# Optimization experiments

Measured on AMD Instinct MI355X. Metric: run time of the kernel, lower is better.

## Reference

```python
import jax, jax.numpy as jnp
import numpy as np

N = 50000          # nodes
E = 1600000        # edges (avg degree 32)
IN_C, HID_C, OUT_C = 256, 256, 256


def setup_inputs() -> dict:
    key = jax.random.key(0)
    ks = jax.random.split(key, 10)
    x = jax.random.normal(ks[0], (N, IN_C), dtype=jnp.float32)
    edge_index = jax.random.randint(ks[1], (2, E), 0, N, dtype=jnp.int32)
    edge_weight = jax.random.uniform(ks[2], (E,), dtype=jnp.float32)
    W1 = jax.random.normal(ks[3], (IN_C, HID_C), dtype=jnp.float32) / np.float32(np.sqrt(IN_C))
    b1 = jnp.zeros((HID_C,), dtype=jnp.float32)
    W2 = jax.random.normal(ks[4], (HID_C, OUT_C), dtype=jnp.float32) / np.float32(np.sqrt(HID_C))
    b2 = jnp.zeros((OUT_C,), dtype=jnp.float32)
    Wf = jax.random.normal(ks[5], (OUT_C, 1), dtype=jnp.float32) / np.float32(np.sqrt(OUT_C))
    bf = jnp.zeros((1,), dtype=jnp.float32)
    return {"x": x, "edge_index": edge_index, "edge_weight": edge_weight,
            "W1": W1, "b1": b1, "W2": W2, "b2": b2, "Wf": Wf, "bf": bf}


def _gcn_norm(edge_index, edge_weight, num_nodes, dtype):
    # add self loops with weight 1 (PyG gcn_norm default, add_self_loops=True)
    src, dst = edge_index[0], edge_index[1]
    loop = jnp.arange(num_nodes, dtype=edge_index.dtype)
    src_f = jnp.concatenate([src, loop])
    dst_f = jnpp_concat = jnp.concatenate([dst, loop])
    w_f = jnp.concatenate([edge_weight.astype(dtype), jnp.ones((num_nodes,), dtype)])
    # degree over destination nodes (flow source_to_target)
    deg = jax.ops.segment_sum(w_f, dst_f, num_segments=num_nodes)
    dinv = jnp.where(deg > 0, jax.lax.rsqrt(deg), jnp.array(0.0, dtype))
    norm = dinv[src_f] * w_f * dinv[dst_f]   # [E + N]
    return src_f, dst_f, norm


def _gcn_conv(x, src_f, dst_f, norm, W, b):
    h = x @ W                                    # transform first: [N, out]
    msg = h[src_f] * norm[:, None]               # gather + edge-wise scale: [E+N, out]
    agg = jax.ops.segment_sum(msg, dst_f, num_segments=x.shape[0])  # scatter-add
    return agg + b


def reference(x, edge_index, edge_weight, W1, b1, W2, b2, Wf, bf):
    n = x.shape[0]
    src_f, dst_f, norm = _gcn_norm(edge_index, edge_weight, n, x.dtype)
    h = jax.nn.relu(_gcn_conv(x, src_f, dst_f, norm, W1, b1))
    h = jax.nn.relu(_gcn_conv(h, src_f, dst_f, norm, W2, b2))
    out = h @ Wf + bf
    return out
```

## Files before the change

kernel.cpp:

```cpp
#include <hip/hip_runtime.h>
#include <hip/hip_bf16.h>
#include <cstdint>

#define IN_C 256

typedef __attribute__((ext_vector_type(8))) short bf16x8;
typedef __attribute__((ext_vector_type(8))) short s16x8;
typedef __attribute__((ext_vector_type(4))) short s16x4;
typedef __attribute__((ext_vector_type(8))) unsigned short u16x8;
typedef __attribute__((ext_vector_type(4))) float f32x4;

#define FIXED_SCALE 33554432.0f
#define FIXED_INV   (1.0f / 33554432.0f)
#define DEG_MASK    ((1ULL << 40) - 1)

__device__ inline unsigned short f2bf(float f) {
    union { float f; unsigned int u; } v; v.f = f;
    unsigned int r = (v.u + 0x7fffu + ((v.u >> 16) & 1u)) >> 16;
    return (unsigned short)r;
}
__device__ inline float bf2f(unsigned short b) {
    union { unsigned int u; float f; } v; v.u = ((unsigned int)b) << 16;
    return v.f;
}
__device__ inline short2 split1(float f) {
    unsigned short hb = f2bf(f);
    unsigned short lb = f2bf(f - bf2f(hb));
    return make_short2((short)hb, (short)lb);
}

__global__ void deg_count_kernel(const int* __restrict__ ei, const float* __restrict__ w,
                                 unsigned long long* __restrict__ packed,
                                 unsigned short* __restrict__ rank, int E) {
    int e = blockIdx.x * blockDim.x + threadIdx.x;
    if (e >= E) return;
    int dst = ei[E + e];
    unsigned int fx = __float2uint_rn(w[e] * FIXED_SCALE);
    unsigned long long inc = (1ULL << 40) | (unsigned long long)fx;
    unsigned long long old = atomicAdd(&packed[dst], inc);
    rank[e] = (unsigned short)(old >> 40);
}

#define SCAN_B 256
__global__ void scan1_kernel(const unsigned long long* __restrict__ packed,
                             int* __restrict__ rp, int* __restrict__ bsum,
                             float* __restrict__ dinv, int N) {
    __shared__ int s[SCAN_B];
    int tid = threadIdx.x;
    int i = blockIdx.x * SCAN_B + tid;
    int v = 0;
    if (i < N) {
        unsigned long long pk = packed[i];
        v = (int)(pk >> 40);
        float deg = (float)(pk & DEG_MASK) * FIXED_INV;
        dinv[i] = rsqrtf(deg + 1.0f);
    }
    s[tid] = v;
    __syncthreads();
    for (int off = 1; off < SCAN_B; off <<= 1) {
        int t = (tid >= off) ? s[tid - off] : 0;
        __syncthreads();
        s[tid] += t;
        __syncthreads();
    }
    if (i < N) rp[i] = s[tid] - v;
    if (tid == SCAN_B - 1) bsum[blockIdx.x] = s[tid];
}

__global__ void scan2_kernel(int* __restrict__ bsum, int* __restrict__ boff, int nb) {
    __shared__ int s[SCAN_B];
    int tid = threadIdx.x;
    int v = (tid < nb) ? bsum[tid] : 0;
    s[tid] = v;
    __syncthreads();
    for (int off = 1; off < SCAN_B; off <<= 1) {
        int t = (tid >= off) ? s[tid - off] : 0;
        __syncthreads();
        s[tid] += t;
        __syncthreads();
    }
    if (tid < nb) boff[tid] = s[tid] - v;
}

__global__ void scan3_kernel(int* __restrict__ rp, const int* __restrict__ boff,
                             int N, int E) {
    int i = blockIdx.x * blockDim.x + threadIdx.x;
    if (i < N) rp[i] = rp[i] + boff[i >> 8];
    if (i == 0) rp[N] = E;
}

__global__ void fill_kernel(const int* __restrict__ ei, const float* __restrict__ w,
                            const float* __restrict__ dinv,
                            const int* __restrict__ rp,
                            const unsigned short* __restrict__ rank,
                            int2* __restrict__ cv, int E) {
    int e = blockIdx.x * blockDim.x + threadIdx.x;
    if (e >= E) return;
    int src = ei[e];
    int dst = ei[E + e];
    int pos = rp[dst] + (int)rank[e];
    if ((unsigned)pos < (unsigned)E) {
        float v = dinv[src] * w[e] * dinv[dst];
        cv[pos] = make_int2(src, __float_as_int(v));
    }
}

__global__ void prep_kernel(const float* __restrict__ W1, const float* __restrict__ W2,
                            const float* __restrict__ x,
                            unsigned short* __restrict__ w1t_hi, unsigned short* __restrict__ w1t_lo,
                            unsigned short* __restrict__ w2t_hi, unsigned short* __restrict__ w2t_lo,
                            unsigned short* __restrict__ x_hi, unsigned short* __restrict__ x_lo,
                            int nx4) {
    int b = blockIdx.x;
    if (b < 512) {
        const float* W = (b < 256) ? W1 : W2;
        unsigned short* hi = (b < 256) ? w1t_hi : w2t_hi;
        unsigned short* lo = (b < 256) ? w1t_lo : w2t_lo;
        int n = b & 255;
        int k = threadIdx.x;
        float v = W[(size_t)k * 256 + n];
        short2 s = split1(v);
        hi[(size_t)n * 256 + k] = (unsigned short)s.x;
        lo[(size_t)n * 256 + k] = (unsigned short)s.y;
    } else {
        int i = (b - 512) * 256 + threadIdx.x;
        if (i < nx4) {
            float4 v = ((const float4*)x)[i];
            short2 sx = split1(v.x), sy = split1(v.y), sz = split1(v.z), sw = split1(v.w);
            s16x4 hv, lv;
            hv.x = sx.x; hv.y = sy.x; hv.z = sz.x; hv.w = sw.x;
            lv.x = sx.y; lv.y = sy.y; lv.z = sz.y; lv.w = sw.y;
            *(s16x4*)(x_hi + (size_t)i * 4) = hv;
            *(s16x4*)(x_lo + (size_t)i * 4) = lv;
        }
    }
}

__global__ __launch_bounds__(256) void gemm_split_kernel(
    const unsigned short* __restrict__ Ahg,
    const unsigned short* __restrict__ Alg,
    const unsigned short* __restrict__ Bth,
    const unsigned short* __restrict__ Btl,
    unsigned short* __restrict__ C16, int Nrows)
{
    __shared__ __align__(16) short Ah[128 * 64];
    __shared__ __align__(16) short Al[128 * 64];
    __shared__ __align__(16) short Bh[128 * 64];
    __shared__ __align__(16) short Bl[128 * 64];

    const int t    = threadIdx.x;
    const int lane = t & 63;
    const int w    = t >> 6;
    const int r0   = blockIdx.x * 128;
    const int cb0  = blockIdx.y * 128;
    const int fr   = lane & 15;
    const int fk   = (lane >> 4) * 8;
    const int wm   = w * 32;

    f32x4 acc[2][8] = {};

    for (int k0 = 0; k0 < 256; k0 += 64) {
        __syncthreads();
#pragma unroll
        for (int c = 0; c < 4; ++c) {
            int i = c * 256 + t;
            int row = i >> 3, seg = i & 7;
            size_t g = (size_t)(cb0 + row) * 256 + k0 + seg * 8;
            *(s16x8*)&Bh[row * 64 + seg * 8] = *(const s16x8*)(Bth + g);
            *(s16x8*)&Bl[row * 64 + seg * 8] = *(const s16x8*)(Btl + g);
        }
#pragma unroll
        for (int c = 0; c < 4; ++c) {
            int i = c * 256 + t;
            int row = i >> 3, seg = i & 7;
            int gr = r0 + row; if (gr > Nrows - 1) gr = Nrows - 1;
            size_t g = (size_t)gr * 256 + k0 + seg * 8;
            *(s16x8*)&Ah[row * 64 + seg * 8] = *(const s16x8*)(Ahg + g);
            *(s16x8*)&Al[row * 64 + seg * 8] = *(const s16x8*)(Alg + g);
        }
        __syncthreads();
#pragma unroll
        for (int ks = 0; ks < 2; ++ks) {
            int ko = ks * 32 + fk;
            bf16x8 ah[2], al[2];
#pragma unroll
            for (int mi = 0; mi < 2; ++mi) {
                ah[mi] = *(const bf16x8*)&Ah[(wm + mi * 16 + fr) * 64 + ko];
                al[mi] = *(const bf16x8*)&Al[(wm + mi * 16 + fr) * 64 + ko];
            }
#pragma unroll
            for (int n = 0; n < 8; ++n) {
                bf16x8 bh = *(const bf16x8*)&Bh[(n * 16 + fr) * 64 + ko];
                bf16x8 bl = *(const bf16x8*)&Bl[(n * 16 + fr) * 64 + ko];
#pragma unroll
                for (int mi = 0; mi < 2; ++mi) {
                    acc[mi][n] = __builtin_amdgcn_mfma_f32_16x16x32_bf16(ah[mi], bh, acc[mi][n], 0, 0, 0);
                    acc[mi][n] = __builtin_amdgcn_mfma_f32_16x16x32_bf16(ah[mi], bl, acc[mi][n], 0, 0, 0);
                    acc[mi][n] = __builtin_amdgcn_mfma_f32_16x16x32_bf16(al[mi], bh, acc[mi][n], 0, 0, 0);
                }
            }
        }
    }
    const int rb = (lane >> 4) * 4;
#pragma unroll
    for (int mi = 0; mi < 2; ++mi) {
#pragma unroll
        for (int n = 0; n < 8; ++n) {
            int col = cb0 + n * 16 + fr;
#pragma unroll
            for (int r = 0; r < 4; ++r) {
                int row = r0 + wm + mi * 16 + rb + r;
                if (row < Nrows) C16[(size_t)row * 256 + col] = f2bf(acc[mi][n][r]);
            }
        }
    }
}

__device__ inline void fma8(float* acc, u16x8 g, float v) {
#pragma unroll
    for (int c = 0; c < 8; ++c) acc[c] = fmaf(v, bf2f(g[c]), acc[c]);
}

__global__ __launch_bounds__(256) void agg_kernel(const unsigned short* __restrict__ h16,
                                                  const int* __restrict__ rp,
                                                  const int2* __restrict__ cv,
                                                  const float* __restrict__ dinv,
                                                  const float* __restrict__ bias,
                                                  unsigned short* __restrict__ out_hi,
                                                  unsigned short* __restrict__ out_lo,
                                                  const float* __restrict__ Wf,
                                                  const float* __restrict__ bf,
                                                  float* __restrict__ out,
                                                  int N) {
    int d    = blockIdx.x * 4 + (threadIdx.x >> 6);
    int lane = threadIdx.x & 63;
    if (d >= N) return;
    int half = lane >> 5;
    int co   = (lane & 31) * 8;

    float di = dinv[d];
    float selfm = half ? 0.0f : di * di;
    u16x8 sv = *(const u16x8*)(h16 + (size_t)d * 256 + co);
    float acc[8];
#pragma unroll
    for (int c = 0; c < 8; ++c) acc[c] = selfm * bf2f(sv[c]);

    int s = rp[d], e = rp[d + 1];
    int j = s;
    for (; j + 16 <= e; j += 16) {
        int   ec[8]; float ev[8];
#pragma unroll
        for (int t2 = 0; t2 < 8; ++t2) {
            int2 ca = cv[j + 2 * t2], cb = cv[j + 2 * t2 + 1];
            ec[t2] = half ? cb.x : ca.x;
            ev[t2] = __int_as_float(half ? cb.y : ca.y);
        }
        u16x8 g0 = *(const u16x8*)(h16 + (size_t)ec[0] * 256 + co);
        u16x8 g1 = *(const u16x8*)(h16 + (size_t)ec[1] * 256 + co);
        u16x8 g2 = *(const u16x8*)(h16 + (size_t)ec[2] * 256 + co);
        u16x8 g3 = *(const u16x8*)(h16 + (size_t)ec[3] * 256 + co);
        u16x8 g4 = *(const u16x8*)(h16 + (size_t)ec[4] * 256 + co);
        u16x8 g5 = *(const u16x8*)(h16 + (size_t)ec[5] * 256 + co);
        u16x8 g6 = *(const u16x8*)(h16 + (size_t)ec[6] * 256 + co);
        u16x8 g7 = *(const u16x8*)(h16 + (size_t)ec[7] * 256 + co);
        fma8(acc, g0, ev[0]);
        fma8(acc, g1, ev[1]);
        fma8(acc, g2, ev[2]);
        fma8(acc, g3, ev[3]);
        fma8(acc, g4, ev[4]);
        fma8(acc, g5, ev[5]);
        fma8(acc, g6, ev[6]);
        fma8(acc, g7, ev[7]);
    }
    for (; j + 8 <= e; j += 8) {
        int   ec[4]; float ev[4];
#pragma unroll
        for (int t2 = 0; t2 < 4; ++t2) {
            int2 ca = cv[j + 2 * t2], cb = cv[j + 2 * t2 + 1];
            ec[t2] = half ? cb.x : ca.x;
            ev[t2] = __int_as_float(half ? cb.y : ca.y);
        }
        u16x8 g0 = *(const u16x8*)(h16 + (size_t)ec[0] * 256 + co);
        u16x8 g1 = *(const u16x8*)(h16 + (size_t)ec[1] * 256 + co);
        u16x8 g2 = *(const u16x8*)(h16 + (size_t)ec[2] * 256 + co);
        u16x8 g3 = *(const u16x8*)(h16 + (size_t)ec[3] * 256 + co);
        fma8(acc, g0, ev[0]);
        fma8(acc, g1, ev[1]);
        fma8(acc, g2, ev[2]);
        fma8(acc, g3, ev[3]);
    }
    for (; j + 2 <= e; j += 2) {
        int2 ca = cv[j], cb = cv[j + 1];
        int   ee = half ? cb.x : ca.x;
        float vv = __int_as_float(half ? cb.y : ca.y);
        u16x8 g = *(const u16x8*)(h16 + (size_t)ee * 256 + co);
        fma8(acc, g, vv);
    }
    if (j < e) {
        int2 ca = cv[j];
        int   ee = ca.x;
        float vv = half ? 0.0f : __int_as_float(ca.y);
        u16x8 g = *(const u16x8*)(h16 + (size_t)ee * 256 + co);
        fma8(acc, g, vv);
    }

#pragma unroll
    for (int c = 0; c < 8; ++c) acc[c] += __shfl_xor(acc[c], 32);

    float4 b0 = *(const float4*)(bias + co);
    float4 b1 = *(const float4*)(bias + co + 4);
    acc[0] = fmaxf(acc[0] + b0.x, 0.0f);
    acc[1] = fmaxf(acc[1] + b0.y, 0.0f);
    acc[2] = fmaxf(acc[2] + b0.z, 0.0f);
    acc[3] = fmaxf(acc[3] + b0.w, 0.0f);
    acc[4] = fmaxf(acc[4] + b1.x, 0.0f);
    acc[5] = fmaxf(acc[5] + b1.y, 0.0f);
    acc[6] = fmaxf(acc[6] + b1.z, 0.0f);
    acc[7] = fmaxf(acc[7] + b1.w, 0.0f);

    if (out_hi != nullptr) {
        u16x8 hi;
#pragma unroll
        for (int c = 0; c < 8; ++c) hi[c] = f2bf(acc[c]);
        if (half == 0) {
            *(u16x8*)(out_hi + (size_t)d * 256 + co) = hi;
        } else {
            u16x8 lo;
#pragma unroll
            for (int c = 0; c < 8; ++c) lo[c] = f2bf(acc[c] - bf2f(hi[c]));
            *(u16x8*)(out_lo + (size_t)d * 256 + co) = lo;
        }
    } else {
        float4 wf0 = *(const float4*)(Wf + co);
        float4 wf1 = *(const float4*)(Wf + co + 4);
        float sdot = acc[0] * wf0.x + acc[1] * wf0.y + acc[2] * wf0.z + acc[3] * wf0.w
                   + acc[4] * wf1.x + acc[5] * wf1.y + acc[6] * wf1.z + acc[7] * wf1.w;
        for (int o = 16; o; o >>= 1) sdot += __shfl_down(sdot, o);
        if (lane == 0) out[d] = sdot + bf[0];
    }
}

extern "C" void kernel_launch(void* const* d_in, const int* in_sizes, int n_in,
                              void* d_out, int out_size, void* d_ws, size_t ws_size,
                              hipStream_t stream) {
    const float* x  = (const float*)d_in[0];
    const int*   ei = (const int*)d_in[1];
    const float* w  = (const float*)d_in[2];
    const float* W1 = (const float*)d_in[3];
    const float* b1 = (const float*)d_in[4];
    const float* W2 = (const float*)d_in[5];
    const float* b2 = (const float*)d_in[6];
    const float* Wf = (const float*)d_in[7];
    const float* bf = (const float*)d_in[8];
    float* out = (float*)d_out;

    const int N = in_sizes[0] / IN_C;
    const int E = in_sizes[2];

    auto align256 = [](size_t v) { return (v + 255) & ~(size_t)255; };
    char* p = (char*)d_ws;
    unsigned long long* packed = (unsigned long long*)p; p += align256((size_t)N * 8);
    float* dinv   = (float*)p; p += align256((size_t)N * 4);
    int*   rp     = (int*)p;   p += align256(((size_t)N + 1) * 4);
    int*   bsum   = (int*)p;   p += align256(SCAN_B * 4);
    int*   boff   = (int*)p;   p += align256(SCAN_B * 4);
    unsigned short* rank = (unsigned short*)p; p += align256((size_t)E * 2);
    int2*  cv     = (int2*)p;  p += align256((size_t)E * 8);
    unsigned short* w1t_hi = (unsigned short*)p; p += align256((size_t)256 * 256 * 2);
    unsigned short* w1t_lo = (unsigned short*)p; p += align256((size_t)256 * 256 * 2);
    unsigned short* w2t_hi = (unsigned short*)p; p += align256((size_t)256 * 256 * 2);
    unsigned short* w2t_lo = (unsigned short*)p; p += align256((size_t)256 * 256 * 2);
    unsigned short* hbuf  = (unsigned short*)p; p += align256((size_t)N * 256 * 2);
    unsigned short* xa_hi = (unsigned short*)p; p += align256((size_t)N * 256 * 2);
    unsigned short* xa_lo = (unsigned short*)p; p += align256((size_t)N * 256 * 2);
    (void)ws_size; (void)n_in; (void)out_size;

    const int nb_edges = (E + 255) / 256;
    const int nb_nodes = (N + 255) / 256;
    const int nb_scan  = (N + SCAN_B - 1) / SCAN_B;
    const int nx4      = N * 256 / 4;

    hipMemsetAsync(packed, 0, (size_t)N * 8, stream);

    deg_count_kernel<<<nb_edges, 256, 0, stream>>>(ei, w, packed, rank, E);
    scan1_kernel<<<nb_scan, SCAN_B, 0, stream>>>(packed, rp, bsum, dinv, N);
    scan2_kernel<<<1, SCAN_B, 0, stream>>>(bsum, boff, nb_scan);
    scan3_kernel<<<nb_nodes, 256, 0, stream>>>(rp, boff, N, E);
    fill_kernel<<<nb_edges, 256, 0, stream>>>(ei, w, dinv, rp, rank, cv, E);

    prep_kernel<<<512 + (nx4 + 255) / 256, 256, 0, stream>>>(
        W1, W2, x, w1t_hi, w1t_lo, w2t_hi, w2t_lo, xa_hi, xa_lo, nx4);

    dim3 ggrid((N + 127) / 128, 2);
    const int nb_agg = (N + 3) / 4;

    gemm_split_kernel<<<ggrid, 256, 0, stream>>>(xa_hi, xa_lo, w1t_hi, w1t_lo, hbuf, N);
    agg_kernel<<<nb_agg, 256, 0, stream>>>(hbuf, rp, cv, dinv, b1,
                                           xa_hi, xa_lo, nullptr, nullptr, nullptr, N);
    gemm_split_kernel<<<ggrid, 256, 0, stream>>>(xa_hi, xa_lo, w2t_hi, w2t_lo, hbuf, N);
    agg_kernel<<<nb_agg, 256, 0, stream>>>(hbuf, rp, cv, dinv, b2,
                                           nullptr, nullptr, Wf, bf, out, N);
}
```

Before: 473.4 us.

## Split aggregation into column slices with four lanes per node

The aggregation kernel now gives each node four lanes covering a 32-column slice, with eight slices launched along grid y. Before, a whole wavefront handled one node with two halves over edges. The goal is to keep each column slice of the gathered feature matrix hot in cache across many nodes and to drop the cross-half shuffle reduction. In exchange, the edge list is re-read eight times, tails are padded with zero-weight gathers, and the final head output needs an extra memset plus an atomicAdd per slice.

```diff
diff --git a/kernel.cpp b/kernel.cpp
--- a/kernel.cpp
+++ b/kernel.cpp
@@ -221,6 +221,7 @@
     for (int c = 0; c < 8; ++c) acc[c] = fmaf(v, bf2f(g[c]), acc[c]);
 }
 
+template<int MODE>
 __global__ __launch_bounds__(256) void agg_kernel(const unsigned short* __restrict__ h16,
                                                   const int* __restrict__ rp,
                                                   const int2* __restrict__ cv,
@@ -232,28 +233,28 @@
                                                   const float* __restrict__ bf,
                                                   float* __restrict__ out,
                                                   int N) {
-    int d    = blockIdx.x * 4 + (threadIdx.x >> 6);
-    int lane = threadIdx.x & 63;
+    int q  = threadIdx.x >> 2;
+    int ql = threadIdx.x & 3;
+    int d  = blockIdx.x * 64 + q;
     if (d >= N) return;
-    int half = lane >> 5;
-    int co   = (lane & 31) * 8;
+    int co = blockIdx.y * 32 + ql * 8;
 
     float di = dinv[d];
-    float selfm = half ? 0.0f : di * di;
+    float selfm = di * di;
     u16x8 sv = *(const u16x8*)(h16 + (size_t)d * 256 + co);
     float acc[8];
 #pragma unroll
     for (int c = 0; c < 8; ++c) acc[c] = selfm * bf2f(sv[c]);
 
     int s = rp[d], e = rp[d + 1];
-    int j = s;
-    for (; j + 16 <= e; j += 16) {
+    for (int j = s; j < e; j += 8) {
         int   ec[8]; float ev[8];
 #pragma unroll
-        for (int t2 = 0; t2 < 8; ++t2) {
-            int2 ca = cv[j + 2 * t2], cb = cv[j + 2 * t2 + 1];
-            ec[t2] = half ? cb.x : ca.x;
-            ev[t2] = __int_as_float(half ? cb.y : ca.y);
+        for (int i = 0; i < 8; ++i) {
+            int idx = j + i;
+            int2 c = cv[idx < e ? idx : e - 1];
+            ec[i] = c.x;
+            ev[i] = (idx < e) ? __int_as_float(c.y) : 0.0f;
         }
         u16x8 g0 = *(const u16x8*)(h16 + (size_t)ec[0] * 256 + co);
         u16x8 g1 = *(const u16x8*)(h16 + (size_t)ec[1] * 256 + co);
@@ -272,40 +273,6 @@
         fma8(acc, g6, ev[6]);
         fma8(acc, g7, ev[7]);
     }
-    for (; j + 8 <= e; j += 8) {
-        int   ec[4]; float ev[4];
-#pragma unroll
-        for (int t2 = 0; t2 < 4; ++t2) {
-            int2 ca = cv[j + 2 * t2], cb = cv[j + 2 * t2 + 1];
-            ec[t2] = half ? cb.x : ca.x;
-            ev[t2] = __int_as_float(half ? cb.y : ca.y);
-        }
-        u16x8 g0 = *(const u16x8*)(h16 + (size_t)ec[0] * 256 + co);
-        u16x8 g1 = *(const u16x8*)(h16 + (size_t)ec[1] * 256 + co);
-        u16x8 g2 = *(const u16x8*)(h16 + (size_t)ec[2] * 256 + co);
-        u16x8 g3 = *(const u16x8*)(h16 + (size_t)ec[3] * 256 + co);
-        fma8(acc, g0, ev[0]);
-        fma8(acc, g1, ev[1]);
-        fma8(acc, g2, ev[2]);
-        fma8(acc, g3, ev[3]);
-    }
-    for (; j + 2 <= e; j += 2) {
-        int2 ca = cv[j], cb = cv[j + 1];
-        int   ee = half ? cb.x : ca.x;
-        float vv = __int_as_float(half ? cb.y : ca.y);
-        u16x8 g = *(const u16x8*)(h16 + (size_t)ee * 256 + co);
-        fma8(acc, g, vv);
-    }
-    if (j < e) {
-        int2 ca = cv[j];
-        int   ee = ca.x;
-        float vv = half ? 0.0f : __int_as_float(ca.y);
-        u16x8 g = *(const u16x8*)(h16 + (size_t)ee * 256 + co);
-        fma8(acc, g, vv);
-    }
-
-#pragma unroll
-    for (int c = 0; c < 8; ++c) acc[c] += __shfl_xor(acc[c], 32);
 
     float4 b0 = *(const float4*)(bias + co);
     float4 b1 = *(const float4*)(bias + co + 4);
@@ -318,25 +285,26 @@
     acc[6] = fmaxf(acc[6] + b1.z, 0.0f);
     acc[7] = fmaxf(acc[7] + b1.w, 0.0f);
 
-    if (out_hi != nullptr) {
-        u16x8 hi;
-#pragma unroll
-        for (int c = 0; c < 8; ++c) hi[c] = f2bf(acc[c]);
-        if (half == 0) {
-            *(u16x8*)(out_hi + (size_t)d * 256 + co) = hi;
-        } else {
-            u16x8 lo;
-#pragma unroll
-            for (int c = 0; c < 8; ++c) lo[c] = f2bf(acc[c] - bf2f(hi[c]));
-            *(u16x8*)(out_lo + (size_t)d * 256 + co) = lo;
-        }
+    if constexpr (MODE == 0) {
+        u16x8 hi, lo;
+#pragma unroll
+        for (int c = 0; c < 8; ++c) {
+            hi[c] = f2bf(acc[c]);
+            lo[c] = f2bf(acc[c] - bf2f(hi[c]));
+        }
+        *(u16x8*)(out_hi + (size_t)d * 256 + co) = hi;
+        *(u16x8*)(out_lo + (size_t)d * 256 + co) = lo;
     } else {
         float4 wf0 = *(const float4*)(Wf + co);
         float4 wf1 = *(const float4*)(Wf + co + 4);
         float sdot = acc[0] * wf0.x + acc[1] * wf0.y + acc[2] * wf0.z + acc[3] * wf0.w
                    + acc[4] * wf1.x + acc[5] * wf1.y + acc[6] * wf1.z + acc[7] * wf1.w;
-        for (int o = 16; o; o >>= 1) sdot += __shfl_down(sdot, o);
-        if (lane == 0) out[d] = sdot + bf[0];
+        sdot += __shfl_xor(sdot, 1);
+        sdot += __shfl_xor(sdot, 2);
+        if (ql == 0) {
+            if (blockIdx.y == 0) sdot += bf[0];
+            atomicAdd(&out[d], sdot);
+        }
     }
 }
 
@@ -381,6 +349,7 @@
     const int nx4      = N * 256 / 4;
 
     hipMemsetAsync(packed, 0, (size_t)N * 8, stream);
+    hipMemsetAsync(out, 0, (size_t)N * 4, stream);
 
     deg_count_kernel<<<nb_edges, 256, 0, stream>>>(ei, w, packed, rank, E);
     scan1_kernel<<<nb_scan, SCAN_B, 0, stream>>>(packed, rp, bsum, dinv, N);
@@ -392,12 +361,12 @@
         W1, W2, x, w1t_hi, w1t_lo, w2t_hi, w2t_lo, xa_hi, xa_lo, nx4);
 
     dim3 ggrid((N + 127) / 128, 2);
-    const int nb_agg = (N + 3) / 4;
+    dim3 agrid((N + 63) / 64, 8);
 
     gemm_split_kernel<<<ggrid, 256, 0, stream>>>(xa_hi, xa_lo, w1t_hi, w1t_lo, hbuf, N);
-    agg_kernel<<<nb_agg, 256, 0, stream>>>(hbuf, rp, cv, dinv, b1,
-                                           xa_hi, xa_lo, nullptr, nullptr, nullptr, N);
+    agg_kernel<0><<<agrid, 256, 0, stream>>>(hbuf, rp, cv, dinv, b1,
+                                             xa_hi, xa_lo, nullptr, nullptr, nullptr, N);
     gemm_split_kernel<<<ggrid, 256, 0, stream>>>(xa_hi, xa_lo, w2t_hi, w2t_lo, hbuf, N);
-    agg_kernel<<<nb_agg, 256, 0, stream>>>(hbuf, rp, cv, dinv, b2,
-                                           nullptr, nullptr, Wf, bf, out, N);
-}
+    agg_kernel<1><<<agrid, 256, 0, stream>>>(hbuf, rp, cv, dinv, b2,
+                                             nullptr, nullptr, Wf, bf, out, N);
+}
```

Result: slower. 582.0 us (+22.9%).
